# Performance work log

Hardware: AMD Instinct MI355X
Metric: run time of the kernel (lower is better)

The kernel has to match this reference:

```python
import jax, jax.numpy as jnp
import numpy as np

B, T, D, H = 4, 2048, 1024, 16
HD = D // H  # head dim = 64


def setup_inputs() -> dict:
    key = jax.random.key(0)
    ks = jax.random.split(key, 9)
    s_in = 1.0 / np.sqrt(D)
    return {
        "token_embedding": jax.random.normal(ks[0], (B, T, D), dtype=jnp.float32),
        # per-head projections, batched over head axis: [H, D, HD]
        "Wq": jax.random.normal(ks[1], (H, D, HD), dtype=jnp.float32) * s_in,
        "bq": jnp.zeros((H, HD), dtype=jnp.float32),
        "Wk": jax.random.normal(ks[2], (H, D, HD), dtype=jnp.float32) * s_in,
        "bk": jnp.zeros((H, HD), dtype=jnp.float32),
        "Wv": jax.random.normal(ks[3], (H, D, HD), dtype=jnp.float32) * s_in,
        "bv": jnp.zeros((H, HD), dtype=jnp.float32),
        "Wo": jax.random.normal(ks[4], (D, D), dtype=jnp.float32) * s_in,
        "bo": jnp.zeros((D,), dtype=jnp.float32),
    }


def _mha(x, Wq, bq, Wk, bk, Wv, bv, Wo, bo):
    # x: [B,T,D]; per-head proj -> [B,H,T,HD]
    q = jnp.einsum('btd,hde->bhte', x, Wq) + bq[None, :, None, :]
    k = jnp.einsum('btd,hde->bhte', x, Wk) + bk[None, :, None, :]
    v = jnp.einsum('btd,hde->bhte', x, Wv) + bv[None, :, None, :]
    scores = jnp.einsum('bhte,bhse->bhts', q, k) / jnp.sqrt(jnp.float32(HD))
    causal = jnp.tril(jnp.ones((T, T), dtype=bool))
    scores = jnp.where(causal[None, None], scores, jnp.float32(-jnp.inf))
    attn = jax.nn.softmax(scores, axis=-1)
    ctx = jnp.einsum('bhts,bhse->bhte', attn, v)  # [B,H,T,HD]
    # concat heads (head order matches ModuleList order) -> [B,T,D]
    cat = jnp.transpose(ctx, (0, 2, 1, 3)).reshape(B, T, D)
    return cat @ Wo + bo


def reference(token_embedding, Wq, bq, Wk, bk, Wv, bv, Wo, bo):
    return _mha(token_embedding, Wq, bq, Wk, bk, Wv, bv, Wo, bo)
```

## Files before the change

### kernel.cpp

```cpp
#include <hip/hip_runtime.h>
#include <hip/hip_bf16.h>
#include <stdint.h>
#include <stddef.h>

#define B_ 4
#define T_ 2048
#define D_ 1024
#define H_ 16
#define HD_ 64
#define LDQKV (3 * D_)

typedef __attribute__((ext_vector_type(8))) __bf16 bf16x8;
typedef __attribute__((ext_vector_type(4))) __bf16 bf16x4;
typedef __attribute__((ext_vector_type(4))) float f32x4;
typedef __attribute__((ext_vector_type(16))) float f32x16;

#define AS1V const __attribute__((address_space(1))) void*
#define AS3V __attribute__((address_space(3))) void*

__global__ void prep_kernel(const float* __restrict__ x, const float* __restrict__ Wq,
                            const float* __restrict__ Wk, const float* __restrict__ Wv,
                            const float* __restrict__ Wo, const float* __restrict__ bq,
                            const float* __restrict__ bk, const float* __restrict__ bv,
                            __bf16* __restrict__ xb, __bf16* __restrict__ wT,
                            __bf16* __restrict__ woT, float* __restrict__ bqkv) {
    const int bid = blockIdx.x, tid = threadIdx.x;
    if (bid < 4096) {
        int i = bid * 256 + tid;
        const float4* p = (const float4*)(x + (size_t)i * 8);
        float4 a = p[0], b = p[1];
        bf16x8 o;
        o[0] = (__bf16)a.x; o[1] = (__bf16)a.y; o[2] = (__bf16)a.z; o[3] = (__bf16)a.w;
        o[4] = (__bf16)b.x; o[5] = (__bf16)b.y; o[6] = (__bf16)b.z; o[7] = (__bf16)b.w;
        *(bf16x8*)(xb + (size_t)i * 8) = o;
    } else if (bid < 16384) {
        int wbid = bid - 4096;
        int which = wbid >> 12;
        int rem = wbid & 4095;
        int h = rem >> 8, z = rem & 255;
        const float* W = (which == 0) ? Wq : (which == 1) ? Wk : Wv;
        int e = tid & 63, dd = tid >> 6;
        float v = W[((size_t)h * D_ + z * 4 + dd) * HD_ + e];
        wT[((size_t)which * D_ + h * HD_ + e) * D_ + z * 4 + dd] = (__bf16)v;
    } else if (bid < 17408) {
        int k = bid - 16384;
        for (int n = tid; n < D_; n += 256)
            woT[(size_t)n * D_ + k] = (__bf16)Wo[(size_t)k * D_ + n];
    } else {
        int n = (bid - 17408) * 256 + tid;
        const float* b = (n < D_) ? bq : (n < 2 * D_) ? bk : bv;
        bqkv[n] = b[n & (D_ - 1)];
    }
}

template <typename OutT, bool SPLITV>
__global__ __launch_bounds__(256, 3)
void gemm_bt_kernel(const __bf16* __restrict__ A, const __bf16* __restrict__ Bt,
                    OutT* __restrict__ C, const float* __restrict__ bias,
                    __bf16* __restrict__ vT,
                    int M, int N, int K, int lda, int ldb, int ldc) {
    __shared__ __bf16 lsA[128 * 64];
    __shared__ __bf16 lsB[128 * 64];
    const int tid = threadIdx.x;
    const int lane = tid & 63;
    const int wave = tid >> 6;
    const int wr = wave >> 1, wc = wave & 1;
    const int lc = lane & 15, lg = lane >> 4;
    const long row0 = (long)blockIdx.y * 128;
    const long col0 = (long)blockIdx.x * 128;

    f32x4 acc[4][4];
#pragma unroll
    for (int mi = 0; mi < 4; mi++)
#pragma unroll
        for (int ni = 0; ni < 4; ni++)
#pragma unroll
            for (int q = 0; q < 4; q++) acc[mi][ni][q] = 0.f;

    const int s_row = tid >> 3, s_k8 = tid & 7;

    for (int k0 = 0; k0 < K; k0 += 64) {
        __syncthreads();
#pragma unroll
        for (int c2 = 0; c2 < 4; c2++) {
            const __bf16* ga = A + (row0 + c2 * 32 + s_row) * (long)lda + k0 + s_k8 * 8;
            const __bf16* gb = Bt + (col0 + c2 * 32 + s_row) * (long)ldb + k0 + s_k8 * 8;
            __bf16* la = lsA + ((c2 << 8) + (wave << 6)) * 8;
            __bf16* lb = lsB + ((c2 << 8) + (wave << 6)) * 8;
            __builtin_amdgcn_global_load_lds((AS1V)ga, (AS3V)la, 16, 0, 0);
            __builtin_amdgcn_global_load_lds((AS1V)gb, (AS3V)lb, 16, 0, 0);
        }
        __syncthreads();
#pragma unroll
        for (int kk = 0; kk < 2; kk++) {
            bf16x8 af[4], bf_[4];
#pragma unroll
            for (int mi = 0; mi < 4; mi++)
                af[mi] = *(const bf16x8*)(lsA + (wr * 64 + mi * 16 + lc) * 64 + (kk * 4 + lg) * 8);
#pragma unroll
            for (int ni = 0; ni < 4; ni++)
                bf_[ni] = *(const bf16x8*)(lsB + (wc * 64 + ni * 16 + lc) * 64 + (kk * 4 + lg) * 8);
#pragma unroll
            for (int mi = 0; mi < 4; mi++)
#pragma unroll
                for (int ni = 0; ni < 4; ni++)
                    acc[mi][ni] =
                        __builtin_amdgcn_mfma_f32_16x16x32_bf16(af[mi], bf_[ni], acc[mi][ni], 0, 0, 0);
        }
    }

    const bool vblock = SPLITV && (col0 >= 2 * D_);
#pragma unroll
    for (int mi = 0; mi < 4; mi++) {
#pragma unroll
        for (int ni = 0; ni < 4; ni++) {
            long r0 = row0 + wr * 64 + mi * 16 + lg * 4;
            long cc = col0 + wc * 64 + ni * 16 + lc;
            float bv = bias[cc];
            if (vblock) {
                long eg = cc - 2 * D_;
                long bb = r0 >> 11;
                long t = r0 & (T_ - 1);
                bf16x4 sv;
#pragma unroll
                for (int q = 0; q < 4; q++) sv[q] = (__bf16)(acc[mi][ni][q] + bv);
                *(bf16x4*)(vT + ((bb << 10) + eg) * T_ + t) = sv;
            } else {
#pragma unroll
                for (int q = 0; q < 4; q++) {
                    float v = acc[mi][ni][q] + bv;
                    C[(r0 + q) * (long)ldc + cc] = (OutT)v;
                }
            }
        }
    }
}

__global__ __launch_bounds__(256, 3)
void attn_kernel(const __bf16* __restrict__ qkv, const __bf16* __restrict__ vT,
                 __bf16* __restrict__ ctx) {
    __shared__ __bf16 lsK[64 * 64];
    __shared__ __bf16 lsV[64 * 64];
    const int tid = threadIdx.x;
    const int lane = tid & 63, w = tid >> 6;
    const int l31 = lane & 31, hi = lane >> 5;
    const int bid = blockIdx.x;
    const int xcd = bid & 7, slot = bid >> 3;
    const int bh = xcd * 8 + (slot & 7);
    const int pr = slot >> 3;
    const int b = bh >> 4, h = bh & 15;
    const float K2 = 0.125f * 1.44269504f;
    const float MBc = 8.0f * K2;

    const __bf16* kbase = qkv + (size_t)(b * T_) * LDQKV + D_ + h * HD_;
    const __bf16* vbase = vT + (size_t)bh * HD_ * T_;

    int s_row[2], s_ch[2];
#pragma unroll
    for (int c2 = 0; c2 < 2; c2++) {
        int idx = c2 * 256 + tid;
        s_row[c2] = idx >> 3;
        s_ch[c2] = idx & 7;
    }

    for (int phase = 0; phase < 2; ++phase) {
        const int chunk = phase ? pr : (15 - pr);
        const int q0 = chunk * 128;
        const int qw = q0 + w * 32;
        const int myq = qw + l31;

        const __bf16* qbase = qkv + (size_t)(b * T_ + myq) * LDQKV + h * HD_;
        bf16x8 qf[4];
#pragma unroll
        for (int kf = 0; kf < 4; kf++) qf[kf] = *(const bf16x8*)(qbase + kf * 16 + hi * 8);

        f32x16 accO[2];
#pragma unroll
        for (int eo = 0; eo < 2; eo++)
#pragma unroll
            for (int r = 0; r < 16; r++) accO[eo][r] = 0.f;
        float l_r = 0.f;

        bf16x8 rK[2], rV[2];
        auto loadKV = [&](int kv0) {
#pragma unroll
            for (int c2 = 0; c2 < 2; c2++) {
                rK[c2] = *(const bf16x8*)(kbase + (size_t)(kv0 + s_row[c2]) * LDQKV + s_ch[c2] * 8);
                rV[c2] = *(const bf16x8*)(vbase + (size_t)s_row[c2] * T_ + kv0 + s_ch[c2] * 8);
            }
        };

        const int ntiles = 2 * (chunk + 1);
        loadKV(0);
        for (int it = 0; it < ntiles; ++it) {
            const int kv0 = it << 6;
            __syncthreads();
#pragma unroll
            for (int c2 = 0; c2 < 2; c2++) {
                *(bf16x8*)(lsK + s_row[c2] * 64 + ((s_ch[c2] ^ (s_row[c2] & 7)) << 3)) = rK[c2];
                *(bf16x8*)(lsV + s_row[c2] * 64 + ((s_ch[c2] ^ (s_row[c2] & 7)) << 3)) = rV[c2];
            }
            __syncthreads();
            if (it + 1 < ntiles) loadKV((it + 1) << 6);

            if (kv0 > qw + 31) continue;

            f32x16 st[2];
            __builtin_amdgcn_s_setprio(1);
#pragma unroll
            for (int kh = 0; kh < 2; kh++) {
                f32x16 a;
#pragma unroll
                for (int r = 0; r < 16; r++) a[r] = 0.f;
#pragma unroll
                for (int kf = 0; kf < 4; kf++) {
                    int row = kh * 32 + l31;
                    int ch = (kf << 1) | hi;
                    bf16x8 kfrag = *(const bf16x8*)(lsK + row * 64 + ((ch ^ (row & 7)) << 3));
                    a = __builtin_amdgcn_mfma_f32_32x32x16_bf16(kfrag, qf[kf], a, 0, 0, 0);
                }
                st[kh] = a;
            }
            __builtin_amdgcn_s_setprio(0);

            if (kv0 + 63 > qw) {
                const int qmk = myq - kv0 - 4 * hi;
#pragma unroll
                for (int kh = 0; kh < 2; kh++)
#pragma unroll
                    for (int r = 0; r < 16; r++) {
                        int kvl = (r & 3) + 8 * (r >> 2) + kh * 32;
                        if (kvl > qmk) st[kh][r] = -1e30f;
                    }
            }

#pragma unroll
            for (int kh = 0; kh < 2; kh++)
#pragma unroll
                for (int r = 0; r < 16; r++) st[kh][r] = exp2f(fmaf(st[kh][r], K2, -MBc));

            float sr[16];
#pragma unroll
            for (int r = 0; r < 16; r++) sr[r] = st[0][r] + st[1][r];
#pragma unroll
            for (int s2 = 8; s2 >= 1; s2 >>= 1)
#pragma unroll
                for (int r = 0; r < s2; r++) sr[r] += sr[r + s2];
            l_r += sr[0] + __shfl_xor(sr[0], 32);

            union BW { unsigned u[4]; bf16x8 v; };
            bf16x8 pfrag[4];
            auto pack2 = [](float a, float b) -> unsigned {
                union { __bf16 h[2]; unsigned u; } x;
                x.h[0] = (__bf16)a;
                x.h[1] = (__bf16)b;
                return x.u;
            };
#pragma unroll
            for (int kh = 0; kh < 2; kh++)
#pragma unroll
                for (int sb = 0; sb < 2; sb++) {
                    int base = sb * 8;
                    unsigned W1 = pack2(st[kh][base + 0], st[kh][base + 1]);
                    unsigned W3 = pack2(st[kh][base + 2], st[kh][base + 3]);
                    unsigned W2 = pack2(st[kh][base + 4], st[kh][base + 5]);
                    unsigned W4 = pack2(st[kh][base + 6], st[kh][base + 7]);
                    unsigned Y1 = hi ? W1 : W2;
                    unsigned Y2 = hi ? W3 : W4;
                    unsigned Z1 = (unsigned)__shfl_xor((int)Y1, 32);
                    unsigned Z2 = (unsigned)__shfl_xor((int)Y2, 32);
                    BW bw;
                    bw.u[0] = hi ? Z1 : W1;
                    bw.u[1] = hi ? Z2 : W3;
                    bw.u[2] = hi ? W2 : Z1;
                    bw.u[3] = hi ? W4 : Z2;
                    pfrag[kh * 2 + sb] = bw.v;
                }

            __builtin_amdgcn_s_setprio(1);
#pragma unroll
            for (int eo = 0; eo < 2; eo++) {
#pragma unroll
                for (int ks = 0; ks < 4; ks++) {
                    int row = eo * 32 + l31;
                    int ch = (ks << 1) | hi;
                    bf16x8 vfrag = *(const bf16x8*)(lsV + row * 64 + ((ch ^ (row & 7)) << 3));
                    accO[eo] = __builtin_amdgcn_mfma_f32_32x32x16_bf16(vfrag, pfrag[ks], accO[eo], 0, 0, 0);
                }
            }
            __builtin_amdgcn_s_setprio(0);
        }

        float invl = 1.0f / l_r;
        __bf16* cb = ctx + (size_t)(b * T_ + myq) * D_ + h * HD_;
#pragma unroll
        for (int eo = 0; eo < 2; eo++)
#pragma unroll
            for (int rg = 0; rg < 4; rg++) {
                bf16x4 sv;
#pragma unroll
                for (int j = 0; j < 4; j++) sv[j] = (__bf16)(accO[eo][rg * 4 + j] * invl);
                *(bf16x4*)(cb + eo * 32 + rg * 8 + 4 * hi) = sv;
            }
    }
}

extern "C" void kernel_launch(void* const* d_in, const int* in_sizes, int n_in,
                              void* d_out, int out_size, void* d_ws, size_t ws_size,
                              hipStream_t stream) {
    const float* x = (const float*)d_in[0];
    const float* Wq = (const float*)d_in[1];
    const float* bq = (const float*)d_in[2];
    const float* Wk = (const float*)d_in[3];
    const float* bk = (const float*)d_in[4];
    const float* Wv = (const float*)d_in[5];
    const float* bv = (const float*)d_in[6];
    const float* Wo = (const float*)d_in[7];
    const float* bo = (const float*)d_in[8];
    float* out = (float*)d_out;

    char* ws = (char*)d_ws;
    size_t off = 0;
    auto alloc = [&](size_t bytes) -> void* {
        off = (off + 255) & ~(size_t)255;
        void* p = ws + off;
        off += bytes;
        return p;
    };
    __bf16* xb = (__bf16*)alloc((size_t)B_ * T_ * D_ * 2);
    __bf16* wT = (__bf16*)alloc((size_t)3 * D_ * D_ * 2);
    float* bqkv = (float*)alloc((size_t)3 * D_ * 4);
    __bf16* woT = (__bf16*)alloc((size_t)D_ * D_ * 2);
    __bf16* qkv = (__bf16*)alloc((size_t)B_ * T_ * 3 * D_ * 2);
    __bf16* vTb = (__bf16*)alloc((size_t)B_ * H_ * HD_ * T_ * 2);
    __bf16* ctx = (__bf16*)alloc((size_t)B_ * T_ * D_ * 2);
    (void)ws_size;
    (void)in_sizes;
    (void)n_in;
    (void)out_size;

    prep_kernel<<<17420, 256, 0, stream>>>(x, Wq, Wk, Wv, Wo, bq, bk, bv, xb, wT, woT, bqkv);

    gemm_bt_kernel<__bf16, true><<<dim3(3 * D_ / 128, B_ * T_ / 128), 256, 0, stream>>>(
        xb, wT, qkv, bqkv, vTb, B_ * T_, 3 * D_, D_, D_, D_, 3 * D_);

    attn_kernel<<<512, 256, 0, stream>>>(qkv, vTb, ctx);

    gemm_bt_kernel<float, false><<<dim3(D_ / 128, B_ * T_ / 128), 256, 0, stream>>>(
        ctx, woT, out, bo, nullptr, B_ * T_, D_, D_, D_, D_, D_);
}
```

Before: 203.2 us.

## Replace QKV projection GEMM with 256x256 eight-wave ping-pong pipelined kernel

Adds a new 512-thread GEMM for the QKV projection. It uses 256x256 output tiles, double-buffered LDS filled by direct global-to-LDS loads with an XOR swizzle, and a fine-grained schedule that interleaves quarter-tile MFMA bursts with the staging of the next K-slice under barriers and priority hints. The aim is higher arithmetic intensity and overlap of memory traffic with MFMA work in the largest GEMM. The cost is 128 KB of LDS per block, fewer blocks (12x32 = 384), and many barriers. The output-projection GEMM keeps the old kernel with the V-split path removed.

```diff
diff --git a/kernel.cpp b/kernel.cpp
--- a/kernel.cpp
+++ b/kernel.cpp
@@ -53,11 +53,167 @@
     }
 }
 
-template <typename OutT, bool SPLITV>
+template <bool SPLITV>
+__global__ __launch_bounds__(512, 2)
+void gemm8p_kernel(const __bf16* __restrict__ A, const __bf16* __restrict__ Bt,
+                   __bf16* __restrict__ C, const float* __restrict__ bias,
+                   __bf16* __restrict__ vT, int lda, int ldb, int ldc) {
+    constexpr int HSZ = 128 * 64;
+    constexpr int TSZ = 2 * HSZ;
+    __shared__ __bf16 lsA[2 * TSZ];
+    __shared__ __bf16 lsB[2 * TSZ];
+    const int tid = threadIdx.x;
+    const int lane = tid & 63, wave = tid >> 6;
+    const int wm = wave >> 2, wn = wave & 3;
+    const int lc = lane & 15, lg = lane >> 4;
+    const long row0 = (long)blockIdx.y * 256;
+    const long col0 = (long)blockIdx.x * 256;
+
+    f32x4 acc[8][4];
+#pragma unroll
+    for (int i = 0; i < 8; i++)
+#pragma unroll
+        for (int jj = 0; jj < 4; jj++)
+#pragma unroll
+            for (int q = 0; q < 4; q++) acc[i][jj][q] = 0.f;
+
+    const int s_row = tid >> 3, s_ch = tid & 7;
+    auto stageA = [&](int t, int d, int h) {
+        long k0 = (long)t * 64;
+#pragma unroll
+        for (int r = 0; r < 2; r++) {
+            int row = r * 64 + s_row;
+            const __bf16* src =
+                A + (row0 + h * 128 + row) * (long)lda + k0 + ((s_ch ^ (row & 7)) << 3);
+            __bf16* dst = lsA + d * TSZ + h * HSZ + (((r << 9) + (tid & ~63)) << 3);
+            __builtin_amdgcn_global_load_lds((AS1V)src, (AS3V)dst, 16, 0, 0);
+        }
+    };
+    auto stageB = [&](int t, int d, int h) {
+        long k0 = (long)t * 64;
+#pragma unroll
+        for (int r = 0; r < 2; r++) {
+            int row = r * 64 + s_row;
+            const __bf16* src =
+                Bt + (col0 + h * 128 + row) * (long)ldb + k0 + ((s_ch ^ (row & 7)) << 3);
+            __bf16* dst = lsB + d * TSZ + h * HSZ + (((r << 9) + (tid & ~63)) << 3);
+            __builtin_amdgcn_global_load_lds((AS1V)src, (AS3V)dst, 16, 0, 0);
+        }
+    };
+
+    bf16x8 af[4][2], bfl[2][2], bfh[2][2];
+    auto readA = [&](int d, int qr) {
+#pragma unroll
+        for (int fr = 0; fr < 4; fr++)
+#pragma unroll
+            for (int kk = 0; kk < 2; kk++) {
+                int row = wm * 128 + qr * 64 + fr * 16 + lc;
+                int ch = (kk * 4 + lg) ^ (row & 7);
+                af[fr][kk] = *(const bf16x8*)(lsA + d * TSZ + row * 64 + ch * 8);
+            }
+    };
+    auto readB = [&](int d, int qc, bf16x8 (*bf)[2]) {
+#pragma unroll
+        for (int fc = 0; fc < 2; fc++)
+#pragma unroll
+            for (int kk = 0; kk < 2; kk++) {
+                int row = wn * 64 + qc * 32 + fc * 16 + lc;
+                int ch = (kk * 4 + lg) ^ (row & 7);
+                bf[fc][kk] = *(const bf16x8*)(lsB + d * TSZ + row * 64 + ch * 8);
+            }
+    };
+    auto mmaQ = [&](int qr, int qc, bf16x8 (*bf)[2]) {
+        __builtin_amdgcn_s_setprio(1);
+#pragma unroll
+        for (int fr = 0; fr < 4; fr++)
+#pragma unroll
+            for (int fc = 0; fc < 2; fc++)
+#pragma unroll
+                for (int kk = 0; kk < 2; kk++)
+                    acc[qr * 4 + fr][qc * 2 + fc] = __builtin_amdgcn_mfma_f32_16x16x32_bf16(
+                        af[fr][kk], bf[fc][kk], acc[qr * 4 + fr][qc * 2 + fc], 0, 0, 0);
+        __builtin_amdgcn_s_setprio(0);
+    };
+
+    stageA(0, 0, 0); stageA(0, 0, 1); stageB(0, 0, 0); stageB(0, 0, 1);
+    stageB(1, 1, 0); stageB(1, 1, 1);
+    asm volatile("s_waitcnt vmcnt(4)\n\ts_barrier" ::: "memory");
+
+    for (int j = 0; j < 8; ++j) {
+        const int x = 2 * j + 2, y = 2 * j + 3, v = 2 * j + 1;
+        const bool more = (j < 7);
+        readA(0, 0); readB(0, 0, bfl);
+        stageA(v, 1, 0);
+        __builtin_amdgcn_s_barrier();
+        mmaQ(0, 0, bfl);
+        __builtin_amdgcn_s_barrier();
+        readB(0, 1, bfh);
+        stageA(v, 1, 1);
+        __builtin_amdgcn_s_barrier();
+        mmaQ(0, 1, bfh);
+        __builtin_amdgcn_s_barrier();
+        readA(0, 1);
+        if (more) stageB(x, 0, 0);
+        __builtin_amdgcn_s_barrier();
+        mmaQ(1, 0, bfl);
+        __builtin_amdgcn_s_barrier();
+        if (more) stageB(x, 0, 1);
+        __builtin_amdgcn_s_barrier();
+        mmaQ(1, 1, bfh);
+        if (more)
+            asm volatile("s_waitcnt vmcnt(4)\n\ts_barrier" ::: "memory");
+        else
+            asm volatile("s_waitcnt vmcnt(0)\n\ts_barrier" ::: "memory");
+        readA(1, 0); readB(1, 0, bfl);
+        if (more) stageA(x, 0, 0);
+        __builtin_amdgcn_s_barrier();
+        mmaQ(0, 0, bfl);
+        __builtin_amdgcn_s_barrier();
+        readB(1, 1, bfh);
+        if (more) stageA(x, 0, 1);
+        __builtin_amdgcn_s_barrier();
+        mmaQ(0, 1, bfh);
+        __builtin_amdgcn_s_barrier();
+        readA(1, 1);
+        if (more) stageB(y, 1, 0);
+        __builtin_amdgcn_s_barrier();
+        mmaQ(1, 0, bfl);
+        __builtin_amdgcn_s_barrier();
+        if (more) stageB(y, 1, 1);
+        __builtin_amdgcn_s_barrier();
+        mmaQ(1, 1, bfh);
+        if (more) asm volatile("s_waitcnt vmcnt(4)\n\ts_barrier" ::: "memory");
+    }
+
+    const bool vblock = SPLITV && (col0 >= 2 * D_);
+#pragma unroll
+    for (int i = 0; i < 8; i++) {
+#pragma unroll
+        for (int jj = 0; jj < 4; jj++) {
+            long r0 = row0 + wm * 128 + (i >> 2) * 64 + (i & 3) * 16 + lg * 4;
+            long cc = col0 + wn * 64 + (jj >> 1) * 32 + (jj & 1) * 16 + lc;
+            float bv = bias[cc];
+            if (vblock) {
+                long eg = cc - 2 * D_;
+                long bb = r0 >> 11;
+                long t = r0 & (T_ - 1);
+                bf16x4 sv;
+#pragma unroll
+                for (int q = 0; q < 4; q++) sv[q] = (__bf16)(acc[i][jj][q] + bv);
+                *(bf16x4*)(vT + ((bb << 10) + eg) * T_ + t) = sv;
+            } else {
+#pragma unroll
+                for (int q = 0; q < 4; q++)
+                    C[(r0 + q) * (long)ldc + cc] = (__bf16)(acc[i][jj][q] + bv);
+            }
+        }
+    }
+}
+
+template <typename OutT>
 __global__ __launch_bounds__(256, 3)
 void gemm_bt_kernel(const __bf16* __restrict__ A, const __bf16* __restrict__ Bt,
                     OutT* __restrict__ C, const float* __restrict__ bias,
-                    __bf16* __restrict__ vT,
                     int M, int N, int K, int lda, int ldb, int ldc) {
     __shared__ __bf16 lsA[128 * 64];
     __shared__ __bf16 lsB[128 * 64];
@@ -109,7 +265,6 @@
         }
     }
 
-    const bool vblock = SPLITV && (col0 >= 2 * D_);
 #pragma unroll
     for (int mi = 0; mi < 4; mi++) {
 #pragma unroll
@@ -117,20 +272,10 @@
             long r0 = row0 + wr * 64 + mi * 16 + lg * 4;
             long cc = col0 + wc * 64 + ni * 16 + lc;
             float bv = bias[cc];
-            if (vblock) {
-                long eg = cc - 2 * D_;
-                long bb = r0 >> 11;
-                long t = r0 & (T_ - 1);
-                bf16x4 sv;
-#pragma unroll
-                for (int q = 0; q < 4; q++) sv[q] = (__bf16)(acc[mi][ni][q] + bv);
-                *(bf16x4*)(vT + ((bb << 10) + eg) * T_ + t) = sv;
-            } else {
-#pragma unroll
-                for (int q = 0; q < 4; q++) {
-                    float v = acc[mi][ni][q] + bv;
-                    C[(r0 + q) * (long)ldc + cc] = (OutT)v;
-                }
+#pragma unroll
+            for (int q = 0; q < 4; q++) {
+                float v = acc[mi][ni][q] + bv;
+                C[(r0 + q) * (long)ldc + cc] = (OutT)v;
             }
         }
     }
@@ -299,7 +444,7 @@
             for (int rg = 0; rg < 4; rg++) {
                 bf16x4 sv;
 #pragma unroll
-                for (int j = 0; j < 4; j++) sv[j] = (__bf16)(accO[eo][rg * 4 + j] * invl);
+                for (int jq = 0; jq < 4; jq++) sv[jq] = (__bf16)(accO[eo][rg * 4 + jq] * invl);
                 *(bf16x4*)(cb + eo * 32 + rg * 8 + 4 * hi) = sv;
             }
     }
@@ -341,11 +486,11 @@
 
     prep_kernel<<<17420, 256, 0, stream>>>(x, Wq, Wk, Wv, Wo, bq, bk, bv, xb, wT, woT, bqkv);
 
-    gemm_bt_kernel<__bf16, true><<<dim3(3 * D_ / 128, B_ * T_ / 128), 256, 0, stream>>>(
-        xb, wT, qkv, bqkv, vTb, B_ * T_, 3 * D_, D_, D_, D_, 3 * D_);
+    gemm8p_kernel<true><<<dim3(3 * D_ / 256, B_ * T_ / 256), 512, 0, stream>>>(
+        xb, wT, qkv, bqkv, vTb, D_, D_, 3 * D_);
 
     attn_kernel<<<512, 256, 0, stream>>>(qkv, vTb, ctx);
 
-    gemm_bt_kernel<float, false><<<dim3(D_ / 128, B_ * T_ / 128), 256, 0, stream>>>(
-        ctx, woT, out, bo, nullptr, B_ * T_, D_, D_, D_, D_, D_);
+    gemm_bt_kernel<float><<<dim3(D_ / 128, B_ * T_ / 128), 256, 0, stream>>>(
+        ctx, woT, out, bo, B_ * T_, D_, D_, D_, D_, D_);
 }
```

After: 204.1 us. Within noise of the previous version (+0.4%).
